# Kernel tuning notes

Measured on AMD Instinct MI355X. Metric: run time of the kernel, lower is better.

Reference implementation:

```python
import jax, jax.numpy as jnp
import numpy as np

L, B = 64, 7          # n_layers, n_bit_options
EPS = 0.02            # sinkhorn entropic regularizer
ITERS = 200           # sinkhorn iterations
TINY = 1e-40


def setup_inputs() -> dict:
    key = jax.random.key(0)
    k1, k2, k3, k4 = jax.random.split(key, 4)
    theta = jax.random.normal(k1, (L, B), dtype=jnp.float32)
    phi = jax.random.normal(k2, (B,), dtype=jnp.float32)
    # layer sizes (param counts), positive; matches layer_sizes buffer usage
    n = jax.random.uniform(k3, (L,), dtype=jnp.float32, minval=4096.0, maxval=262144.0)
    sens = jax.random.uniform(k4, (L,), dtype=jnp.float32)
    sens = sens / sens.sum()  # update_sensitivity normalizes to a distribution
    bits = jnp.arange(2, 2 + B, dtype=jnp.float32)
    err = 2.0 ** (-2.0 * bits)  # quantization error per bitwidth
    return {"theta": theta, "phi": phi, "n": n, "sens": sens, "err": err}


def reference(theta, phi, n, sens, err):
    # DiffAllocator.compute_P
    a = n / n.sum()                         # row marginal (buffer 'a')
    b = jax.nn.softmax(phi)                 # col marginal b()
    C = (n * sens)[:, None] * err[None, :]  # build_cost: [L,B]
    K = -(C - theta) / EPS                  # log-kernel
    log_a = jnp.log(a + TINY)
    log_b = jnp.log(b + TINY)
    f0 = jnp.zeros((L,), dtype=theta.dtype)
    g0 = jnp.zeros((B,), dtype=theta.dtype)

    def step(carry, _):
        f, g = carry
        f = log_a - jax.scipy.special.logsumexp(K + g[None, :], axis=1)
        g = log_b - jax.scipy.special.logsumexp(K + f[:, None], axis=0)
        return (f, g), None

    (f, g), _ = jax.lax.scan(step, (f0, g0), None, length=ITERS)
    P = jnp.exp(K + f[:, None] + g[None, :])
    return P / (P.sum() + TINY)
```

## Files before the change

### kernel.cpp

```cpp
#include <hip/hip_runtime.h>
#include <math.h>

#define NB 7
#define EPS_ 0.02f
#define ITERS_ 200
#define TINY_ 1e-40f
#define GTOL_ 2e-5f
#define LOG2E_ 1.4426950408889634f
#define LN2_   0.6931471805599453f

__device__ __forceinline__ float exp2_hw(float x) {
#if __has_builtin(__builtin_amdgcn_exp2f)
    return __builtin_amdgcn_exp2f(x);
#else
    return __expf(x * LN2_);
#endif
}
__device__ __forceinline__ float log2_hw(float x) {
#if __has_builtin(__builtin_amdgcn_logf)
    return __builtin_amdgcn_logf(x);
#else
    return __logf(x) * LOG2E_;
#endif
}

template <int CTRL>
__device__ __forceinline__ float dpp_ident(float identity, float x) {
    return __int_as_float(__builtin_amdgcn_update_dpp(
        __float_as_int(identity), __float_as_int(x), CTRL, 0xF, 0xF, false));
}
__device__ __forceinline__ float readlane63(float x) {
    return __int_as_float(__builtin_amdgcn_readlane(__float_as_int(x), 63));
}
__device__ __forceinline__ float wave_sum_bcast(float s) {
    s += dpp_ident<0x111>(0.f, s);
    s += dpp_ident<0x112>(0.f, s);
    s += dpp_ident<0x114>(0.f, s);
    s += dpp_ident<0x118>(0.f, s);
    s += dpp_ident<0x142>(0.f, s);
    s += dpp_ident<0x143>(0.f, s);
    return readlane63(s);
}
__device__ __forceinline__ float wave_max_bcast(float m) {
    const float NI = __int_as_float(0xff800000);
    m = fmaxf(m, dpp_ident<0x111>(NI, m));
    m = fmaxf(m, dpp_ident<0x112>(NI, m));
    m = fmaxf(m, dpp_ident<0x114>(NI, m));
    m = fmaxf(m, dpp_ident<0x118>(NI, m));
    m = fmaxf(m, dpp_ident<0x142>(NI, m));
    m = fmaxf(m, dpp_ident<0x143>(NI, m));
    return readlane63(m);
}

#define WAVE_MAX7(v0,v1,v2,v3,v4,v5,v6, m0,m1,m2,m3,m4,m5,m6)                 \
  {                                                                           \
    float r0,r1,r2,r3,r4,r5,r6;                                               \
    asm("v_mov_b32 %0, %14\n\t"                                               \
        "v_mov_b32 %1, %15\n\t"                                               \
        "v_mov_b32 %2, %16\n\t"                                               \
        "v_mov_b32 %3, %17\n\t"                                               \
        "v_mov_b32 %4, %18\n\t"                                               \
        "v_mov_b32 %5, %19\n\t"                                               \
        "v_mov_b32 %6, %20\n\t"                                               \
        "v_max_f32_dpp %0, %0, %0 row_shr:1 row_mask:0xf bank_mask:0xf\n\t"   \
        "v_max_f32_dpp %1, %1, %1 row_shr:1 row_mask:0xf bank_mask:0xf\n\t"   \
        "v_max_f32_dpp %2, %2, %2 row_shr:1 row_mask:0xf bank_mask:0xf\n\t"   \
        "v_max_f32_dpp %3, %3, %3 row_shr:1 row_mask:0xf bank_mask:0xf\n\t"   \
        "v_max_f32_dpp %4, %4, %4 row_shr:1 row_mask:0xf bank_mask:0xf\n\t"   \
        "v_max_f32_dpp %5, %5, %5 row_shr:1 row_mask:0xf bank_mask:0xf\n\t"   \
        "v_max_f32_dpp %6, %6, %6 row_shr:1 row_mask:0xf bank_mask:0xf\n\t"   \
        "v_max_f32_dpp %0, %0, %0 row_shr:2 row_mask:0xf bank_mask:0xf\n\t"   \
        "v_max_f32_dpp %1, %1, %1 row_shr:2 row_mask:0xf bank_mask:0xf\n\t"   \
        "v_max_f32_dpp %2, %2, %2 row_shr:2 row_mask:0xf bank_mask:0xf\n\t"   \
        "v_max_f32_dpp %3, %3, %3 row_shr:2 row_mask:0xf bank_mask:0xf\n\t"   \
        "v_max_f32_dpp %4, %4, %4 row_shr:2 row_mask:0xf bank_mask:0xf\n\t"   \
        "v_max_f32_dpp %5, %5, %5 row_shr:2 row_mask:0xf bank_mask:0xf\n\t"   \
        "v_max_f32_dpp %6, %6, %6 row_shr:2 row_mask:0xf bank_mask:0xf\n\t"   \
        "v_max_f32_dpp %0, %0, %0 row_shr:4 row_mask:0xf bank_mask:0xf\n\t"   \
        "v_max_f32_dpp %1, %1, %1 row_shr:4 row_mask:0xf bank_mask:0xf\n\t"   \
        "v_max_f32_dpp %2, %2, %2 row_shr:4 row_mask:0xf bank_mask:0xf\n\t"   \
        "v_max_f32_dpp %3, %3, %3 row_shr:4 row_mask:0xf bank_mask:0xf\n\t"   \
        "v_max_f32_dpp %4, %4, %4 row_shr:4 row_mask:0xf bank_mask:0xf\n\t"   \
        "v_max_f32_dpp %5, %5, %5 row_shr:4 row_mask:0xf bank_mask:0xf\n\t"   \
        "v_max_f32_dpp %6, %6, %6 row_shr:4 row_mask:0xf bank_mask:0xf\n\t"   \
        "v_max_f32_dpp %0, %0, %0 row_shr:8 row_mask:0xf bank_mask:0xf\n\t"   \
        "v_max_f32_dpp %1, %1, %1 row_shr:8 row_mask:0xf bank_mask:0xf\n\t"   \
        "v_max_f32_dpp %2, %2, %2 row_shr:8 row_mask:0xf bank_mask:0xf\n\t"   \
        "v_max_f32_dpp %3, %3, %3 row_shr:8 row_mask:0xf bank_mask:0xf\n\t"   \
        "v_max_f32_dpp %4, %4, %4 row_shr:8 row_mask:0xf bank_mask:0xf\n\t"   \
        "v_max_f32_dpp %5, %5, %5 row_shr:8 row_mask:0xf bank_mask:0xf\n\t"   \
        "v_max_f32_dpp %6, %6, %6 row_shr:8 row_mask:0xf bank_mask:0xf\n\t"   \
        "v_max_f32_dpp %0, %0, %0 row_bcast:15 row_mask:0xa bank_mask:0xf\n\t"\
        "v_max_f32_dpp %1, %1, %1 row_bcast:15 row_mask:0xa bank_mask:0xf\n\t"\
        "v_max_f32_dpp %2, %2, %2 row_bcast:15 row_mask:0xa bank_mask:0xf\n\t"\
        "v_max_f32_dpp %3, %3, %3 row_bcast:15 row_mask:0xa bank_mask:0xf\n\t"\
        "v_max_f32_dpp %4, %4, %4 row_bcast:15 row_mask:0xa bank_mask:0xf\n\t"\
        "v_max_f32_dpp %5, %5, %5 row_bcast:15 row_mask:0xa bank_mask:0xf\n\t"\
        "v_max_f32_dpp %6, %6, %6 row_bcast:15 row_mask:0xa bank_mask:0xf\n\t"\
        "v_max_f32_dpp %0, %0, %0 row_bcast:31 row_mask:0xc bank_mask:0xf\n\t"\
        "v_max_f32_dpp %1, %1, %1 row_bcast:31 row_mask:0xc bank_mask:0xf\n\t"\
        "v_max_f32_dpp %2, %2, %2 row_bcast:31 row_mask:0xc bank_mask:0xf\n\t"\
        "v_max_f32_dpp %3, %3, %3 row_bcast:31 row_mask:0xc bank_mask:0xf\n\t"\
        "v_max_f32_dpp %4, %4, %4 row_bcast:31 row_mask:0xc bank_mask:0xf\n\t"\
        "v_max_f32_dpp %5, %5, %5 row_bcast:31 row_mask:0xc bank_mask:0xf\n\t"\
        "v_max_f32_dpp %6, %6, %6 row_bcast:31 row_mask:0xc bank_mask:0xf\n\t"\
        "v_readlane_b32 %7, %0, 63\n\t"                                       \
        "v_readlane_b32 %8, %1, 63\n\t"                                       \
        "v_readlane_b32 %9, %2, 63\n\t"                                       \
        "v_readlane_b32 %10, %3, 63\n\t"                                      \
        "v_readlane_b32 %11, %4, 63\n\t"                                      \
        "v_readlane_b32 %12, %5, 63\n\t"                                      \
        "v_readlane_b32 %13, %6, 63\n\t"                                      \
        "s_nop 1"                                                             \
        : "=&v"(r0), "=&v"(r1), "=&v"(r2), "=&v"(r3),                         \
          "=&v"(r4), "=&v"(r5), "=&v"(r6),                                    \
          "=s"(m0), "=s"(m1), "=s"(m2), "=s"(m3),                             \
          "=s"(m4), "=s"(m5), "=s"(m6)                                        \
        : "v"(v0), "v"(v1), "v"(v2), "v"(v3), "v"(v4), "v"(v5), "v"(v6));     \
  }

#define WAVE_SUM7(e0,e1,e2,e3,e4,e5,e6, s0_,s1_,s2_,s3_,s4_,s5_,s6_)          \
    asm("s_nop 1\n\t"                                                         \
        "v_add_f32_dpp %0, %0, %0 row_shr:1 row_mask:0xf bank_mask:0xf\n\t"   \
        "v_add_f32_dpp %1, %1, %1 row_shr:1 row_mask:0xf bank_mask:0xf\n\t"   \
        "v_add_f32_dpp %2, %2, %2 row_shr:1 row_mask:0xf bank_mask:0xf\n\t"   \
        "v_add_f32_dpp %3, %3, %3 row_shr:1 row_mask:0xf bank_mask:0xf\n\t"   \
        "v_add_f32_dpp %4, %4, %4 row_shr:1 row_mask:0xf bank_mask:0xf\n\t"   \
        "v_add_f32_dpp %5, %5, %5 row_shr:1 row_mask:0xf bank_mask:0xf\n\t"   \
        "v_add_f32_dpp %6, %6, %6 row_shr:1 row_mask:0xf bank_mask:0xf\n\t"   \
        "v_add_f32_dpp %0, %0, %0 row_shr:2 row_mask:0xf bank_mask:0xf\n\t"   \
        "v_add_f32_dpp %1, %1, %1 row_shr:2 row_mask:0xf bank_mask:0xf\n\t"   \
        "v_add_f32_dpp %2, %2, %2 row_shr:2 row_mask:0xf bank_mask:0xf\n\t"   \
        "v_add_f32_dpp %3, %3, %3 row_shr:2 row_mask:0xf bank_mask:0xf\n\t"   \
        "v_add_f32_dpp %4, %4, %4 row_shr:2 row_mask:0xf bank_mask:0xf\n\t"   \
        "v_add_f32_dpp %5, %5, %5 row_shr:2 row_mask:0xf bank_mask:0xf\n\t"   \
        "v_add_f32_dpp %6, %6, %6 row_shr:2 row_mask:0xf bank_mask:0xf\n\t"   \
        "v_add_f32_dpp %0, %0, %0 row_shr:4 row_mask:0xf bank_mask:0xf\n\t"   \
        "v_add_f32_dpp %1, %1, %1 row_shr:4 row_mask:0xf bank_mask:0xf\n\t"   \
        "v_add_f32_dpp %2, %2, %2 row_shr:4 row_mask:0xf bank_mask:0xf\n\t"   \
        "v_add_f32_dpp %3, %3, %3 row_shr:4 row_mask:0xf bank_mask:0xf\n\t"   \
        "v_add_f32_dpp %4, %4, %4 row_shr:4 row_mask:0xf bank_mask:0xf\n\t"   \
        "v_add_f32_dpp %5, %5, %5 row_shr:4 row_mask:0xf bank_mask:0xf\n\t"   \
        "v_add_f32_dpp %6, %6, %6 row_shr:4 row_mask:0xf bank_mask:0xf\n\t"   \
        "v_add_f32_dpp %0, %0, %0 row_shr:8 row_mask:0xf bank_mask:0xf\n\t"   \
        "v_add_f32_dpp %1, %1, %1 row_shr:8 row_mask:0xf bank_mask:0xf\n\t"   \
        "v_add_f32_dpp %2, %2, %2 row_shr:8 row_mask:0xf bank_mask:0xf\n\t"   \
        "v_add_f32_dpp %3, %3, %3 row_shr:8 row_mask:0xf bank_mask:0xf\n\t"   \
        "v_add_f32_dpp %4, %4, %4 row_shr:8 row_mask:0xf bank_mask:0xf\n\t"   \
        "v_add_f32_dpp %5, %5, %5 row_shr:8 row_mask:0xf bank_mask:0xf\n\t"   \
        "v_add_f32_dpp %6, %6, %6 row_shr:8 row_mask:0xf bank_mask:0xf\n\t"   \
        "v_add_f32_dpp %0, %0, %0 row_bcast:15 row_mask:0xa bank_mask:0xf\n\t"\
        "v_add_f32_dpp %1, %1, %1 row_bcast:15 row_mask:0xa bank_mask:0xf\n\t"\
        "v_add_f32_dpp %2, %2, %2 row_bcast:15 row_mask:0xa bank_mask:0xf\n\t"\
        "v_add_f32_dpp %3, %3, %3 row_bcast:15 row_mask:0xa bank_mask:0xf\n\t"\
        "v_add_f32_dpp %4, %4, %4 row_bcast:15 row_mask:0xa bank_mask:0xf\n\t"\
        "v_add_f32_dpp %5, %5, %5 row_bcast:15 row_mask:0xa bank_mask:0xf\n\t"\
        "v_add_f32_dpp %6, %6, %6 row_bcast:15 row_mask:0xa bank_mask:0xf\n\t"\
        "v_add_f32_dpp %0, %0, %0 row_bcast:31 row_mask:0xc bank_mask:0xf\n\t"\
        "v_add_f32_dpp %1, %1, %1 row_bcast:31 row_mask:0xc bank_mask:0xf\n\t"\
        "v_add_f32_dpp %2, %2, %2 row_bcast:31 row_mask:0xc bank_mask:0xf\n\t"\
        "v_add_f32_dpp %3, %3, %3 row_bcast:31 row_mask:0xc bank_mask:0xf\n\t"\
        "v_add_f32_dpp %4, %4, %4 row_bcast:31 row_mask:0xc bank_mask:0xf\n\t"\
        "v_add_f32_dpp %5, %5, %5 row_bcast:31 row_mask:0xc bank_mask:0xf\n\t"\
        "v_add_f32_dpp %6, %6, %6 row_bcast:31 row_mask:0xc bank_mask:0xf\n\t"\
        "v_readlane_b32 %7, %0, 63\n\t"                                       \
        "v_readlane_b32 %8, %1, 63\n\t"                                       \
        "v_readlane_b32 %9, %2, 63\n\t"                                       \
        "v_readlane_b32 %10, %3, 63\n\t"                                      \
        "v_readlane_b32 %11, %4, 63\n\t"                                      \
        "v_readlane_b32 %12, %5, 63\n\t"                                      \
        "v_readlane_b32 %13, %6, 63\n\t"                                      \
        "s_nop 1"                                                             \
        : "+v"(e0), "+v"(e1), "+v"(e2), "+v"(e3),                             \
          "+v"(e4), "+v"(e5), "+v"(e6),                                       \
          "=s"(s0_), "=s"(s1_), "=s"(s2_), "=s"(s3_),                         \
          "=s"(s4_), "=s"(s5_), "=s"(s6_))

__global__ __launch_bounds__(64) void sinkhorn_kernel(
    const float* __restrict__ theta,
    const float* __restrict__ phi,
    const float* __restrict__ n,
    const float* __restrict__ sens,
    const float* __restrict__ err,
    float* __restrict__ out)
{
    const int lane = threadIdx.x;

    const float ni = n[lane];
    const float si = sens[lane];

    const float kscale = LOG2E_ / EPS_;
    float K2[NB];
    #pragma unroll
    for (int j = 0; j < NB; ++j)
        K2[j] = (theta[lane * NB + j] - ni * si * err[j]) * kscale;

    const float nsum   = wave_sum_bcast(ni);
    const float log_a2 = log2_hw(ni / nsum + TINY_);

    float t2[NB];
    #pragma unroll
    for (int j = 0; j < NB; ++j) t2[j] = phi[j] * LOG2E_;
    float pmax = t2[0];
    #pragma unroll
    for (int j = 1; j < NB; ++j) pmax = fmaxf(pmax, t2[j]);
    float psum = 0.f;
    #pragma unroll
    for (int j = 0; j < NB; ++j) psum += exp2_hw(t2[j] - pmax);
    const float lps = log2_hw(psum);
    float log_b2[NB], KB2[NB];
    #pragma unroll
    for (int j = 0; j < NB; ++j) {
        log_b2[j] = log2_hw(exp2_hw(t2[j] - pmax - lps) + TINY_);
        KB2[j]    = K2[j] + log_b2[j];
    }

    float lse[NB], prev[NB];
    #pragma unroll
    for (int j = 0; j < NB; ++j) { lse[j] = log_b2[j]; prev[j] = lse[j]; }

    float f2 = 0.f;
    int okcnt = 0;
    const unsigned LO = 0x0D800000u;
    const unsigned HI = 0x71800000u;

    for (int t = 1; t <= ITERS_; ++t) {
        float w[NB];
        #pragma unroll
        for (int j = 0; j < NB; ++j) w[j] = KB2[j] - lse[j];
        const float m = fmaxf(fmaxf(fmaxf(w[0], w[1]), fmaxf(w[2], w[3])),
                              fmaxf(fmaxf(w[4], w[5]), w[6]));
        float s = 0.f;
        #pragma unroll
        for (int j = 0; j < NB; ++j) s += exp2_hw(w[j] - m);
        f2 = log_a2 - (m + log2_hw(s));

        float v0 = K2[0] + f2, v1 = K2[1] + f2, v2 = K2[2] + f2,
              v3 = K2[3] + f2, v4 = K2[4] + f2, v5 = K2[5] + f2,
              v6 = K2[6] + f2;
        float e0 = exp2_hw(v0 - lse[0]), e1 = exp2_hw(v1 - lse[1]),
              e2 = exp2_hw(v2 - lse[2]), e3 = exp2_hw(v3 - lse[3]),
              e4 = exp2_hw(v4 - lse[4]), e5 = exp2_hw(v5 - lse[5]),
              e6 = exp2_hw(v6 - lse[6]);
        float ss0, ss1, ss2, ss3, ss4, ss5, ss6;
        WAVE_SUM7(e0, e1, e2, e3, e4, e5, e6, ss0, ss1, ss2, ss3, ss4, ss5, ss6);

        const unsigned u0 = __float_as_uint(ss0), u1 = __float_as_uint(ss1),
                       u2 = __float_as_uint(ss2), u3 = __float_as_uint(ss3),
                       u4 = __float_as_uint(ss4), u5 = __float_as_uint(ss5),
                       u6 = __float_as_uint(ss6);
        const unsigned umin = min(min(min(u0, u1), min(u2, u3)),
                                  min(min(u4, u5), u6));
        const unsigned umax = max(max(max(u0, u1), max(u2, u3)),
                                  max(max(u4, u5), u6));
        if (umin < LO || umax > HI) {
            float mm0, mm1, mm2, mm3, mm4, mm5, mm6;
            WAVE_MAX7(v0, v1, v2, v3, v4, v5, v6, mm0, mm1, mm2, mm3, mm4, mm5, mm6);
            e0 = exp2_hw(v0 - mm0); e1 = exp2_hw(v1 - mm1);
            e2 = exp2_hw(v2 - mm2); e3 = exp2_hw(v3 - mm3);
            e4 = exp2_hw(v4 - mm4); e5 = exp2_hw(v5 - mm5);
            e6 = exp2_hw(v6 - mm6);
            WAVE_SUM7(e0, e1, e2, e3, e4, e5, e6, ss0, ss1, ss2, ss3, ss4, ss5, ss6);
            lse[0] = mm0 + log2_hw(ss0); lse[1] = mm1 + log2_hw(ss1);
            lse[2] = mm2 + log2_hw(ss2); lse[3] = mm3 + log2_hw(ss3);
            lse[4] = mm4 + log2_hw(ss4); lse[5] = mm5 + log2_hw(ss5);
            lse[6] = mm6 + log2_hw(ss6);
        } else {
            lse[0] += log2_hw(ss0); lse[1] += log2_hw(ss1);
            lse[2] += log2_hw(ss2); lse[3] += log2_hw(ss3);
            lse[4] += log2_hw(ss4); lse[5] += log2_hw(ss5);
            lse[6] += log2_hw(ss6);
        }

        if ((t & 1) == 0) {
            float d = fabsf(lse[0] - prev[0]);
            #pragma unroll
            for (int j = 1; j < NB; ++j) d = fmaxf(d, fabsf(lse[j] - prev[j]));
            #pragma unroll
            for (int j = 0; j < NB; ++j) prev[j] = lse[j];
            okcnt = (d < GTOL_ && t > 16) ? okcnt + 1 : 0;
            if (okcnt >= 2) break;
        }
    }

    const float NI = __int_as_float(0xff800000);
    float x[NB];
    float m = NI;
    #pragma unroll
    for (int j = 0; j < NB; ++j) {
        x[j] = K2[j] + f2 + (log_b2[j] - lse[j]);
        m = fmaxf(m, x[j]);
    }
    m = wave_max_bcast(m);

    float p[NB];
    float s = 0.f;
    #pragma unroll
    for (int j = 0; j < NB; ++j) {
        p[j] = exp2_hw(x[j] - m);
        s += p[j];
    }
    s = wave_sum_bcast(s);

    const float inv = 1.0f / (s + exp2_hw(-132.87712379549449f - m));
    #pragma unroll
    for (int j = 0; j < NB; ++j)
        out[lane * NB + j] = p[j] * inv;
}

extern "C" void kernel_launch(void* const* d_in, const int* in_sizes, int n_in,
                              void* d_out, int out_size, void* d_ws, size_t ws_size,
                              hipStream_t stream) {
    const float* theta = (const float*)d_in[0];
    const float* phi   = (const float*)d_in[1];
    const float* n     = (const float*)d_in[2];
    const float* sens  = (const float*)d_in[3];
    const float* err   = (const float*)d_in[4];
    float* out = (float*)d_out;

    sinkhorn_kernel<<<1, 64, 0, stream>>>(theta, phi, n, sens, err, out);
}
```

Before: 137.5 us.

## Reformulate Sinkhorn loop on a single potential-shifted state and drop early exit

Rewrites the Sinkhorn iteration to carry one combined log-state t = K + f - lse per element, so the row logsumexp skips the per-row max subtraction whenever every lane's sum is in range (checked with a wave ballot) and only falls back to the stable path otherwise. It also removes the convergence check, so the loop now always runs the full 200 iterations. This trims exp/max work per iteration, but the missing early exit may add iterations when the old check would have stopped sooner.

```diff
diff --git a/kernel.cpp b/kernel.cpp
--- a/kernel.cpp
+++ b/kernel.cpp
@@ -5,7 +5,6 @@
 #define EPS_ 0.02f
 #define ITERS_ 200
 #define TINY_ 1e-40f
-#define GTOL_ 2e-5f
 #define LOG2E_ 1.4426950408889634f
 #define LN2_   0.6931471805599453f
 
@@ -198,50 +197,55 @@
     const float nsum   = wave_sum_bcast(ni);
     const float log_a2 = log2_hw(ni / nsum + TINY_);
 
-    float t2[NB];
-    #pragma unroll
-    for (int j = 0; j < NB; ++j) t2[j] = phi[j] * LOG2E_;
-    float pmax = t2[0];
-    #pragma unroll
-    for (int j = 1; j < NB; ++j) pmax = fmaxf(pmax, t2[j]);
+    float t2v[NB];
+    #pragma unroll
+    for (int j = 0; j < NB; ++j) t2v[j] = phi[j] * LOG2E_;
+    float pmax = t2v[0];
+    #pragma unroll
+    for (int j = 1; j < NB; ++j) pmax = fmaxf(pmax, t2v[j]);
     float psum = 0.f;
     #pragma unroll
-    for (int j = 0; j < NB; ++j) psum += exp2_hw(t2[j] - pmax);
+    for (int j = 0; j < NB; ++j) psum += exp2_hw(t2v[j] - pmax);
     const float lps = log2_hw(psum);
-    float log_b2[NB], KB2[NB];
+    float log_b2[NB], cb[NB];
     #pragma unroll
     for (int j = 0; j < NB; ++j) {
-        log_b2[j] = log2_hw(exp2_hw(t2[j] - pmax - lps) + TINY_);
-        KB2[j]    = K2[j] + log_b2[j];
+        log_b2[j] = log2_hw(exp2_hw(t2v[j] - pmax - lps) + TINY_);
+        cb[j]     = log_b2[j] - log_a2;
     }
 
-    float lse[NB], prev[NB];
-    #pragma unroll
-    for (int j = 0; j < NB; ++j) { lse[j] = log_b2[j]; prev[j] = lse[j]; }
-
-    float f2 = 0.f;
-    int okcnt = 0;
-    const unsigned LO = 0x0D800000u;
-    const unsigned HI = 0x71800000u;
-
-    for (int t = 1; t <= ITERS_; ++t) {
-        float w[NB];
-        #pragma unroll
-        for (int j = 0; j < NB; ++j) w[j] = KB2[j] - lse[j];
-        const float m = fmaxf(fmaxf(fmaxf(w[0], w[1]), fmaxf(w[2], w[3])),
-                              fmaxf(fmaxf(w[4], w[5]), w[6]));
-        float s = 0.f;
-        #pragma unroll
-        for (int j = 0; j < NB; ++j) s += exp2_hw(w[j] - m);
-        f2 = log_a2 - (m + log2_hw(s));
-
-        float v0 = K2[0] + f2, v1 = K2[1] + f2, v2 = K2[2] + f2,
-              v3 = K2[3] + f2, v4 = K2[4] + f2, v5 = K2[5] + f2,
-              v6 = K2[6] + f2;
-        float e0 = exp2_hw(v0 - lse[0]), e1 = exp2_hw(v1 - lse[1]),
-              e2 = exp2_hw(v2 - lse[2]), e3 = exp2_hw(v3 - lse[3]),
-              e4 = exp2_hw(v4 - lse[4]), e5 = exp2_hw(v5 - lse[5]),
-              e6 = exp2_hw(v6 - lse[6]);
+    float t[NB];
+    #pragma unroll
+    for (int j = 0; j < NB; ++j) t[j] = K2[j] - log_b2[j];
+
+    const float LOF = __int_as_float(0x0D800000);
+    const float HIF = __int_as_float(0x71800000);
+    const unsigned LO = 0x0D800000u, HI = 0x71800000u;
+
+    for (int it = 0; it < ITERS_; ++it) {
+        float a0 = t[0] + cb[0], a1 = t[1] + cb[1], a2 = t[2] + cb[2],
+              a3 = t[3] + cb[3], a4 = t[4] + cb[4], a5 = t[5] + cb[5],
+              a6 = t[6] + cb[6];
+        float s = ((exp2_hw(a0) + exp2_hw(a1)) + (exp2_hw(a2) + exp2_hw(a3)))
+                + ((exp2_hw(a4) + exp2_hw(a5)) + exp2_hw(a6));
+        float L;
+        const bool ok = (s >= LOF) && (s <= HIF);
+        if (__ballot(ok) == ~0ull) {
+            L = log2_hw(s);
+        } else {
+            float m = fmaxf(fmaxf(fmaxf(a0, a1), fmaxf(a2, a3)),
+                            fmaxf(fmaxf(a4, a5), a6));
+            float s2 = ((exp2_hw(a0 - m) + exp2_hw(a1 - m))
+                      + (exp2_hw(a2 - m) + exp2_hw(a3 - m)))
+                     + ((exp2_hw(a4 - m) + exp2_hw(a5 - m)) + exp2_hw(a6 - m));
+            L = m + log2_hw(s2);
+        }
+
+        float q0 = t[0] - L, q1 = t[1] - L, q2 = t[2] - L, q3 = t[3] - L,
+              q4 = t[4] - L, q5 = t[5] - L, q6 = t[6] - L;
+        float e0 = exp2_hw(q0), e1 = exp2_hw(q1), e2 = exp2_hw(q2),
+              e3 = exp2_hw(q3), e4 = exp2_hw(q4), e5 = exp2_hw(q5),
+              e6 = exp2_hw(q6);
         float ss0, ss1, ss2, ss3, ss4, ss5, ss6;
         WAVE_SUM7(e0, e1, e2, e3, e4, e5, e6, ss0, ss1, ss2, ss3, ss4, ss5, ss6);
 
@@ -254,32 +258,22 @@
         const unsigned umax = max(max(max(u0, u1), max(u2, u3)),
                                   max(max(u4, u5), u6));
         if (umin < LO || umax > HI) {
-            float mm0, mm1, mm2, mm3, mm4, mm5, mm6;
-            WAVE_MAX7(v0, v1, v2, v3, v4, v5, v6, mm0, mm1, mm2, mm3, mm4, mm5, mm6);
-            e0 = exp2_hw(v0 - mm0); e1 = exp2_hw(v1 - mm1);
-            e2 = exp2_hw(v2 - mm2); e3 = exp2_hw(v3 - mm3);
-            e4 = exp2_hw(v4 - mm4); e5 = exp2_hw(v5 - mm5);
-            e6 = exp2_hw(v6 - mm6);
+            float M0, M1, M2, M3, M4, M5, M6;
+            WAVE_MAX7(q0, q1, q2, q3, q4, q5, q6, M0, M1, M2, M3, M4, M5, M6);
+            e0 = exp2_hw(q0 - M0); e1 = exp2_hw(q1 - M1);
+            e2 = exp2_hw(q2 - M2); e3 = exp2_hw(q3 - M3);
+            e4 = exp2_hw(q4 - M4); e5 = exp2_hw(q5 - M5);
+            e6 = exp2_hw(q6 - M6);
             WAVE_SUM7(e0, e1, e2, e3, e4, e5, e6, ss0, ss1, ss2, ss3, ss4, ss5, ss6);
-            lse[0] = mm0 + log2_hw(ss0); lse[1] = mm1 + log2_hw(ss1);
-            lse[2] = mm2 + log2_hw(ss2); lse[3] = mm3 + log2_hw(ss3);
-            lse[4] = mm4 + log2_hw(ss4); lse[5] = mm5 + log2_hw(ss5);
-            lse[6] = mm6 + log2_hw(ss6);
+            t[0] = q0 - (M0 + log2_hw(ss0)); t[1] = q1 - (M1 + log2_hw(ss1));
+            t[2] = q2 - (M2 + log2_hw(ss2)); t[3] = q3 - (M3 + log2_hw(ss3));
+            t[4] = q4 - (M4 + log2_hw(ss4)); t[5] = q5 - (M5 + log2_hw(ss5));
+            t[6] = q6 - (M6 + log2_hw(ss6));
         } else {
-            lse[0] += log2_hw(ss0); lse[1] += log2_hw(ss1);
-            lse[2] += log2_hw(ss2); lse[3] += log2_hw(ss3);
-            lse[4] += log2_hw(ss4); lse[5] += log2_hw(ss5);
-            lse[6] += log2_hw(ss6);
-        }
-
-        if ((t & 1) == 0) {
-            float d = fabsf(lse[0] - prev[0]);
-            #pragma unroll
-            for (int j = 1; j < NB; ++j) d = fmaxf(d, fabsf(lse[j] - prev[j]));
-            #pragma unroll
-            for (int j = 0; j < NB; ++j) prev[j] = lse[j];
-            okcnt = (d < GTOL_ && t > 16) ? okcnt + 1 : 0;
-            if (okcnt >= 2) break;
+            t[0] = q0 - log2_hw(ss0); t[1] = q1 - log2_hw(ss1);
+            t[2] = q2 - log2_hw(ss2); t[3] = q3 - log2_hw(ss3);
+            t[4] = q4 - log2_hw(ss4); t[5] = q5 - log2_hw(ss5);
+            t[6] = q6 - log2_hw(ss6);
         }
     }
 
@@ -288,7 +282,7 @@
     float m = NI;
     #pragma unroll
     for (int j = 0; j < NB; ++j) {
-        x[j] = K2[j] + f2 + (log_b2[j] - lse[j]);
+        x[j] = t[j] + log_b2[j];
         m = fmaxf(m, x[j]);
     }
     m = wave_max_bcast(m);
```

Result: faster. 123.2 us (-10.4%).
